# Optimization experiments

Hardware: AMD Instinct MI355X
Metric: run time of the kernel (lower is better)

## Reference

```python
import jax, jax.numpy as jnp
import numpy as np

B, S, D = 4, 2048, 1024
P = 2
N_FEAT = 16          # n_feature_know
N_REST = 16          # n_restore_know
R = 128              # knowledge_rank
D_SPACE = 64


def setup_inputs() -> dict:
    key = jax.random.key(0)
    ks = jax.random.split(key, 6)
    x = jax.random.normal(ks[0], (B, S, D), dtype=jnp.float32)
    # per-token routing weights for each of P feature paths, in [0,1)
    feature_paths = jax.random.uniform(ks[1], (P, B, S, N_FEAT), dtype=jnp.float32)
    f_know = jax.random.normal(ks[2], (N_FEAT, D, R), dtype=jnp.float32) * 0.02
    r_know = jax.random.normal(ks[3], (N_REST, R, D), dtype=jnp.float32) * 0.02
    feature_emb = jax.random.normal(ks[4], (N_FEAT, D_SPACE), dtype=jnp.float32)
    W_router = jax.random.normal(ks[5], (D_SPACE + R, N_REST), dtype=jnp.float32) * 0.05
    return {"x": x, "feature_paths": feature_paths, "f_know": f_know,
            "r_know": r_know, "feature_emb": feature_emb, "W_router": W_router}


def reference(x, feature_paths, f_know, r_know, feature_emb, W_router):
    # Feature projection into all N low-rank banks: [B,S,N,R]
    all_h = jnp.einsum('bsd,ndr->bsnr', x, f_know)
    # Weighted sum over banks per path: [P,B,S,R]
    h_all = jnp.einsum('bsnr,pbsn->pbsr', all_h, feature_paths)
    # Context for restore routing: [P,B,S,D_SPACE]
    neuron_ctx = jnp.einsum('pbsn,nd->pbsd', feature_paths, feature_emb)
    # restore_input = cat([neuron_ctx, h]) -> router -> softmax restore weights
    restore_input = jnp.concatenate([neuron_ctx, h_all], axis=-1)  # [P,B,S,D_SPACE+R]
    logits = jnp.einsum('pbsc,cn->pbsn', restore_input, W_router)
    w = jax.nn.softmax(logits, axis=-1)                            # [P,B,S,N_REST]
    # Restore + per-token weighted combine, summed over P paths: [B,S,D]
    output = jnp.einsum('pbsr,nrd,pbsn->bsd', h_all, r_know, w)
    restore_aux_loss = jnp.float32(0.0)
    return output, restore_aux_loss
```

## Files before the change

kernel.cpp:

```cpp
#include <hip/hip_runtime.h>

typedef __attribute__((ext_vector_type(4))) float f32x4;
typedef __bf16 bf16x8 __attribute__((ext_vector_type(8)));
typedef unsigned short ushort_t;

#define T_TOK 8192
#define DIM   1024
#define NRCOL 2048

#define VMW(n)  asm volatile("s_waitcnt vmcnt(" #n ")" ::: "memory")
#define SB0()   __builtin_amdgcn_sched_barrier(0)
#define BAR()   __builtin_amdgcn_s_barrier()

static __device__ __forceinline__ unsigned short f2bf(float f) {
  unsigned int u = __builtin_bit_cast(unsigned int, f);
  u += 0x7fffu + ((u >> 16) & 1u);
  return (unsigned short)(u >> 16);
}
static __device__ __forceinline__ float bfbits2f(unsigned int lo16) {
  return __builtin_bit_cast(float, lo16 << 16);
}
static __device__ __forceinline__ void gload16(const void* g, void* l) {
  __builtin_amdgcn_global_load_lds((const __attribute__((address_space(1))) void*)g,
                                   (__attribute__((address_space(3))) void*)l, 16, 0, 0);
}

__global__ __launch_bounds__(256) void cvt_f32_bf16(const float* __restrict__ in,
                                                    unsigned short* __restrict__ out,
                                                    int n4) {
  int i = blockIdx.x * 256 + threadIdx.x;
  const int stride = gridDim.x * 256;
  const float4* in4 = (const float4*)in;
  uint2* o4 = (uint2*)out;
  for (; i < n4; i += stride) {
    float4 v = in4[i];
    uint2 o;
    o.x = (unsigned)f2bf(v.x) | ((unsigned)f2bf(v.y) << 16);
    o.y = (unsigned)f2bf(v.z) | ((unsigned)f2bf(v.w) << 16);
    o4[i] = o;
  }
}

__global__ __launch_bounds__(256) void tcvt(const float* __restrict__ src,
                                            unsigned short* __restrict__ dst,
                                            int rows, int cols,
                                            long sstride, long dstride) {
  src += (size_t)blockIdx.z * sstride;
  dst += (size_t)blockIdx.z * dstride;
  __shared__ float tile[32][33];
  const int tx = threadIdx.x & 31, ty = threadIdx.x >> 5;
  const int r0 = blockIdx.y * 32, c0 = blockIdx.x * 32;
  #pragma unroll
  for (int i = 0; i < 32; i += 8)
    tile[ty + i][tx] = src[(size_t)(r0 + ty + i) * cols + c0 + tx];
  __syncthreads();
  #pragma unroll
  for (int i = 0; i < 32; i += 8)
    dst[(size_t)(c0 + ty + i) * rows + r0 + tx] = f2bf(tile[tx][ty + i]);
}

template<int BM, int BK, int K, bool OUT_BF16>
__global__ __launch_bounds__(512, 2) void gemmP(const ushort_t* __restrict__ A,
                                                const ushort_t* __restrict__ Bt,
                                                void* __restrict__ Cp, int N) {
  constexpr int nt = K / BK;
  constexpr int KS = BK / 32;
  constexpr int MF = BM / 32;
  constexpr int CH = BK / 8;
  constexpr int AR = BM * BK * 2 / 8192;
  constexpr int BR = 256 * BK * 2 / 8192;
  constexpr int LPT = AR + BR;
  __shared__ ushort_t As[3][BM * BK];
  __shared__ ushort_t Bs[3][256 * BK];

  const int tid = threadIdx.x;
  const int nx = gridDim.x;
  const int orig = blockIdx.y * nx + blockIdx.x;
  const int q = (nx * gridDim.y) >> 3;
  const int swz = (orig & 7) * q + (orig >> 3);
  const int bx = swz % nx, by = swz / nx;

  const int lane = tid & 63, wv = tid >> 6;
  const int wm = wv >> 2, wn = wv & 3;
  const int lrow = lane & 15, lk = lane >> 4;

  const ushort_t* Ab = A + (size_t)by * BM * K;
  const ushort_t* Bb = Bt + (size_t)bx * 256 * K;

  const int srow = tid * 16 / (BK * 2);
  const int sch = ((tid * 16 >> 4) & (CH - 1)) ^ (srow & (CH - 1));
  constexpr int RPR = 8192 / (BK * 2);
  const ushort_t* pA[AR];
  const ushort_t* pB[BR];
  #pragma unroll
  for (int r = 0; r < AR; ++r) pA[r] = Ab + (size_t)(r * RPR + srow) * K + sch * 8;
  #pragma unroll
  for (int r = 0; r < BR; ++r) pB[r] = Bb + (size_t)(r * RPR + srow) * K + sch * 8;
  const int dL = tid * 8;

  int oA[MF], oB[4];
  #pragma unroll
  for (int m = 0; m < MF; ++m) {
    const int r = wm * (BM / 2) + m * 16 + lrow;
    oA[m] = r * BK + (lk ^ (r & (CH - 1))) * 8;
  }
  #pragma unroll
  for (int n = 0; n < 4; ++n) {
    const int r = wn * 64 + n * 16 + lrow;
    oB[n] = r * BK + (lk ^ (r & (CH - 1))) * 8;
  }

  f32x4 acc[MF][4];
  #pragma unroll
  for (int m = 0; m < MF; ++m)
    #pragma unroll
    for (int n = 0; n < 4; ++n)
      acc[m][n] = (f32x4){0.f, 0.f, 0.f, 0.f};

  auto stage = [&](int s, int adv) {
    #pragma unroll
    for (int r = 0; r < AR; ++r) gload16(pA[r] + adv, (void*)&As[s][r * 4096 + dL]);
    #pragma unroll
    for (int r = 0; r < BR; ++r) gload16(pB[r] + adv, (void*)&Bs[s][r * 4096 + dL]);
  };

  stage(0, 0);
  stage(1, BK);
  if constexpr (LPT == 4) VMW(4); else VMW(6);
  SB0(); BAR(); SB0();

  bf16x8 av[2][MF][KS], bv01[2][KS], bv23[2][KS];
  #pragma unroll
  for (int m = 0; m < MF; ++m)
    #pragma unroll
    for (int ks = 0; ks < KS; ++ks)
      av[0][m][ks] = *(const bf16x8*)&As[0][oA[m] ^ (ks * 32)];
  #pragma unroll
  for (int n = 0; n < 2; ++n)
    #pragma unroll
    for (int ks = 0; ks < KS; ++ks)
      bv01[n][ks] = *(const bf16x8*)&Bs[0][oB[n] ^ (ks * 32)];

  #pragma unroll
  for (int t = 0; t < nt; ++t) {
    const int s = t % 3, s1 = (t + 1) % 3, s2 = (t + 2) % 3;
    const int p = t & 1;
    if (t + 2 < nt) stage(s2, (t + 2) * BK);
    #pragma unroll
    for (int n = 0; n < 2; ++n)
      #pragma unroll
      for (int ks = 0; ks < KS; ++ks)
        bv23[n][ks] = *(const bf16x8*)&Bs[s][oB[n + 2] ^ (ks * 32)];
    #pragma unroll
    for (int ks = 0; ks < KS; ++ks)
      #pragma unroll
      for (int m = 0; m < MF; ++m)
        #pragma unroll
        for (int n = 0; n < 2; ++n)
          acc[m][n] = __builtin_amdgcn_mfma_f32_16x16x32_bf16(av[p][m][ks], bv01[n][ks], acc[m][n], 0, 0, 0);
    SB0();
    if (t + 2 < nt) { if constexpr (LPT == 4) VMW(4); else VMW(6); }
    else            { VMW(0); }
    BAR(); SB0();
    if (t + 1 < nt) {
      #pragma unroll
      for (int m = 0; m < MF; ++m)
        #pragma unroll
        for (int ks = 0; ks < KS; ++ks)
          av[p ^ 1][m][ks] = *(const bf16x8*)&As[s1][oA[m] ^ (ks * 32)];
      #pragma unroll
      for (int n = 0; n < 2; ++n)
        #pragma unroll
        for (int ks = 0; ks < KS; ++ks)
          bv01[n][ks] = *(const bf16x8*)&Bs[s1][oB[n] ^ (ks * 32)];
    }
    #pragma unroll
    for (int ks = 0; ks < KS; ++ks)
      #pragma unroll
      for (int m = 0; m < MF; ++m)
        #pragma unroll
        for (int n = 0; n < 2; ++n)
          acc[m][n + 2] = __builtin_amdgcn_mfma_f32_16x16x32_bf16(av[p][m][ks], bv23[n][ks], acc[m][n + 2], 0, 0, 0);
    SB0(); BAR(); SB0();
  }

  #pragma unroll
  for (int m = 0; m < MF; ++m) {
    const int row0 = by * BM + wm * (BM / 2) + m * 16 + lk * 4;
    #pragma unroll
    for (int n = 0; n < 4; ++n) {
      const int col = bx * 256 + wn * 64 + n * 16 + lrow;
      #pragma unroll
      for (int j = 0; j < 4; ++j) {
        const size_t idx = (size_t)(row0 + j) * N + col;
        if constexpr (OUT_BF16) ((ushort_t*)Cp)[idx] = f2bf(acc[m][n][j]);
        else                    ((float*)Cp)[idx] = acc[m][n][j];
      }
    }
  }
}

__global__ __launch_bounds__(256) void middle_kernel(const unsigned short* __restrict__ AH,
                                                     const float* __restrict__ fp,
                                                     const float* __restrict__ femb,
                                                     const float* __restrict__ Wr,
                                                     unsigned short* __restrict__ Mout,
                                                     float* __restrict__ auxout) {
  __shared__ float G[16][16];
  __shared__ float hs[4][2][128];
  __shared__ float wsm[4][2][16];
  const int tid = threadIdx.x;
  {
    const int n = tid >> 4, j = tid & 15;
    float s = 0.f;
    #pragma unroll
    for (int ds = 0; ds < 64; ++ds) s += femb[n * 64 + ds] * Wr[ds * 16 + j];
    G[n][j] = s;
  }
  const int wv = tid >> 6, l = tid & 63;
  const int t = blockIdx.x * 4 + wv;

  float p0[16], p1[16];
  #pragma unroll
  for (int n = 0; n < 16; ++n) {
    p0[n] = fp[t * 16 + n];
    p1[n] = fp[T_TOK * 16 + t * 16 + n];
  }

  float h00 = 0.f, h01 = 0.f, h10 = 0.f, h11 = 0.f;
  const unsigned short* ahrow = AH + (size_t)t * NRCOL;
  #pragma unroll
  for (int n = 0; n < 16; ++n) {
    const unsigned int v = *(const unsigned int*)(ahrow + n * 128 + 2 * l);
    const float a0 = bfbits2f(v & 0xffffu);
    const float a1 = bfbits2f(v >> 16);
    h00 += a0 * p0[n]; h01 += a1 * p0[n];
    h10 += a0 * p1[n]; h11 += a1 * p1[n];
  }
  hs[wv][0][2 * l] = h00; hs[wv][0][2 * l + 1] = h01;
  hs[wv][1][2 * l] = h10; hs[wv][1][2 * l + 1] = h11;
  __syncthreads();

  if (l < 32) {
    const int p = l >> 4, j = l & 15;
    float s = 0.f;
    #pragma unroll
    for (int n = 0; n < 16; ++n) s += (p ? p1[n] : p0[n]) * G[n][j];
    const float* hp = hs[wv][p];
    const float* wr = Wr + 64 * 16 + j;
    float s0 = 0.f, s1 = 0.f, s2 = 0.f, s3 = 0.f;
    #pragma unroll
    for (int r = 0; r < 128; r += 4) {
      s0 += hp[r]     * wr[(r)     * 16];
      s1 += hp[r + 1] * wr[(r + 1) * 16];
      s2 += hp[r + 2] * wr[(r + 2) * 16];
      s3 += hp[r + 3] * wr[(r + 3) * 16];
    }
    s += (s0 + s1) + (s2 + s3);
    float mx = s;
    #pragma unroll
    for (int d = 1; d < 16; d <<= 1) mx = fmaxf(mx, __shfl_xor(mx, d, 64));
    const float e = __expf(s - mx);
    float sum = e;
    #pragma unroll
    for (int d = 1; d < 16; d <<= 1) sum += __shfl_xor(sum, d, 64);
    wsm[wv][p][j] = e / sum;
  }
  __syncthreads();

  unsigned short* mrow = Mout + (size_t)t * NRCOL;
  #pragma unroll
  for (int n = 0; n < 16; ++n) {
    const float w0 = wsm[wv][0][n], w1 = wsm[wv][1][n];
    const float m0 = w0 * h00 + w1 * h10;
    const float m1 = w0 * h01 + w1 * h11;
    const unsigned int pk = (unsigned)f2bf(m0) | ((unsigned)f2bf(m1) << 16);
    *(unsigned int*)(mrow + n * 128 + 2 * l) = pk;
  }
  if (blockIdx.x == 0 && tid == 0) auxout[0] = 0.f;
}

extern "C" void kernel_launch(void* const* d_in, const int* in_sizes, int n_in,
                              void* d_out, int out_size, void* d_ws, size_t ws_size,
                              hipStream_t stream) {
  const float* x    = (const float*)d_in[0];
  const float* fp   = (const float*)d_in[1];
  const float* fk   = (const float*)d_in[2];
  const float* rk   = (const float*)d_in[3];
  const float* femb = (const float*)d_in[4];
  const float* Wr   = (const float*)d_in[5];
  float* out = (float*)d_out;

  char* ws = (char*)d_ws;
  unsigned short* Xbf = (unsigned short*)ws;
  unsigned short* W1t = (unsigned short*)(ws + 16u * 1024 * 1024);
  unsigned short* Mb  = (unsigned short*)ws;
  unsigned short* W2t = (unsigned short*)(ws + 32u * 1024 * 1024);
  unsigned short* AH  = (unsigned short*)(ws + 36u * 1024 * 1024);

  cvt_f32_bf16<<<2048, 256, 0, stream>>>(x, Xbf, (T_TOK * DIM) / 4);
  tcvt<<<dim3(128 / 32, 1024 / 32, 16), 256, 0, stream>>>(fk, W1t, 1024, 128,
                                                          1024L * 128, 128L * 1024);
  tcvt<<<dim3(1024 / 32, 2048 / 32, 1), 256, 0, stream>>>(rk, W2t, 2048, 1024, 0, 0);
  gemmP<256, 32, 1024, true><<<dim3(NRCOL / 256, T_TOK / 256), 512, 0, stream>>>(Xbf, W1t, AH, NRCOL);
  middle_kernel<<<T_TOK / 4, 256, 0, stream>>>(AH, fp, femb, Wr, Mb, out + 8388608);
  gemmP<128, 64, 2048, false><<<dim3(DIM / 256, T_TOK / 128), 512, 0, stream>>>(Mb, W2t, out, DIM);
}
```

Before: 115.9 us.

## Fuse prep conversions into one kernel, retile first GEMM, parallelize router logits

Merges the x bf16 conversion and the two weight transpose-conversions into a single prep kernel launch, which removes two launch gaps. Switches the first GEMM tile from BM=256/BK=32 to BM=128/BK=64, doubling its grid for better occupancy and load balance. In the middle kernel, the router weights are staged in shared memory and all 64 lanes compute the logits, with the rank dimension split across two half-wavefronts and combined by a shuffle instead of only 32 lanes reading global memory. The cost is extra shared memory and a larger preload per block in the middle kernel.

```diff
diff --git a/kernel.cpp b/kernel.cpp
--- a/kernel.cpp
+++ b/kernel.cpp
@@ -25,31 +25,45 @@
                                    (__attribute__((address_space(3))) void*)l, 16, 0, 0);
 }
 
-__global__ __launch_bounds__(256) void cvt_f32_bf16(const float* __restrict__ in,
-                                                    unsigned short* __restrict__ out,
-                                                    int n4) {
-  int i = blockIdx.x * 256 + threadIdx.x;
-  const int stride = gridDim.x * 256;
-  const float4* in4 = (const float4*)in;
-  uint2* o4 = (uint2*)out;
-  for (; i < n4; i += stride) {
-    float4 v = in4[i];
-    uint2 o;
-    o.x = (unsigned)f2bf(v.x) | ((unsigned)f2bf(v.y) << 16);
-    o.y = (unsigned)f2bf(v.z) | ((unsigned)f2bf(v.w) << 16);
-    o4[i] = o;
-  }
-}
-
-__global__ __launch_bounds__(256) void tcvt(const float* __restrict__ src,
-                                            unsigned short* __restrict__ dst,
-                                            int rows, int cols,
-                                            long sstride, long dstride) {
-  src += (size_t)blockIdx.z * sstride;
-  dst += (size_t)blockIdx.z * dstride;
+__global__ __launch_bounds__(256) void prep_kernel(const float* __restrict__ x,
+                                                   const float* __restrict__ fk,
+                                                   const float* __restrict__ rk,
+                                                   unsigned short* __restrict__ Xbf,
+                                                   unsigned short* __restrict__ W1t,
+                                                   unsigned short* __restrict__ W2t) {
+  const int bid = blockIdx.x, tid = threadIdx.x;
+  if (bid < 2048) {
+    const float4* in4 = (const float4*)x;
+    uint2* o4 = (uint2*)Xbf;
+    #pragma unroll
+    for (int it = 0; it < 4; ++it) {
+      const int i = bid * 256 + tid + it * 524288;
+      float4 v = in4[i];
+      uint2 o;
+      o.x = (unsigned)f2bf(v.x) | ((unsigned)f2bf(v.y) << 16);
+      o.y = (unsigned)f2bf(v.z) | ((unsigned)f2bf(v.w) << 16);
+      o4[i] = o;
+    }
+    return;
+  }
   __shared__ float tile[32][33];
-  const int tx = threadIdx.x & 31, ty = threadIdx.x >> 5;
-  const int r0 = blockIdx.y * 32, c0 = blockIdx.x * 32;
+  const float* src;
+  unsigned short* dst;
+  int rows, cols, r0, c0;
+  if (bid < 4096) {
+    const int b = bid - 2048;
+    const int z = b >> 7, rem = b & 127;
+    src = fk + (size_t)z * 1024 * 128;
+    dst = W1t + (size_t)z * 128 * 1024;
+    rows = 1024; cols = 128;
+    c0 = (rem & 3) * 32; r0 = (rem >> 2) * 32;
+  } else {
+    const int b = bid - 4096;
+    src = rk; dst = W2t;
+    rows = 2048; cols = 1024;
+    c0 = (b & 31) * 32; r0 = (b >> 5) * 32;
+  }
+  const int tx = tid & 31, ty = tid >> 5;
   #pragma unroll
   for (int i = 0; i < 32; i += 8)
     tile[ty + i][tx] = src[(size_t)(r0 + ty + i) * cols + c0 + tx];
@@ -207,6 +221,7 @@
                                                      unsigned short* __restrict__ Mout,
                                                      float* __restrict__ auxout) {
   __shared__ float G[16][16];
+  __shared__ float WrBs[128 * 16];
   __shared__ float hs[4][2][128];
   __shared__ float wsm[4][2][16];
   const int tid = threadIdx.x;
@@ -216,6 +231,9 @@
     #pragma unroll
     for (int ds = 0; ds < 64; ++ds) s += femb[n * 64 + ds] * Wr[ds * 16 + j];
     G[n][j] = s;
+    #pragma unroll
+    for (int k = 0; k < 8; ++k)
+      WrBs[tid * 8 + k] = Wr[64 * 16 + tid * 8 + k];
   }
   const int wv = tid >> 6, l = tid & 63;
   const int t = blockIdx.x * 4 + wv;
@@ -241,22 +259,25 @@
   hs[wv][1][2 * l] = h10; hs[wv][1][2 * l + 1] = h11;
   __syncthreads();
 
-  if (l < 32) {
-    const int p = l >> 4, j = l & 15;
-    float s = 0.f;
-    #pragma unroll
-    for (int n = 0; n < 16; ++n) s += (p ? p1[n] : p0[n]) * G[n][j];
-    const float* hp = hs[wv][p];
-    const float* wr = Wr + 64 * 16 + j;
+  {
+    const int p = l >> 5, seg = (l >> 4) & 1, j = l & 15;
+    const float* hp = hs[wv][p] + seg * 64;
+    const float* wb = WrBs + seg * 64 * 16 + j;
     float s0 = 0.f, s1 = 0.f, s2 = 0.f, s3 = 0.f;
     #pragma unroll
-    for (int r = 0; r < 128; r += 4) {
-      s0 += hp[r]     * wr[(r)     * 16];
-      s1 += hp[r + 1] * wr[(r + 1) * 16];
-      s2 += hp[r + 2] * wr[(r + 2) * 16];
-      s3 += hp[r + 3] * wr[(r + 3) * 16];
-    }
-    s += (s0 + s1) + (s2 + s3);
+    for (int r = 0; r < 64; r += 4) {
+      s0 += hp[r]     * wb[(r)     * 16];
+      s1 += hp[r + 1] * wb[(r + 1) * 16];
+      s2 += hp[r + 2] * wb[(r + 2) * 16];
+      s3 += hp[r + 3] * wb[(r + 3) * 16];
+    }
+    float s = (s0 + s1) + (s2 + s3);
+    s += __shfl_xor(s, 16, 64);
+    #pragma unroll
+    for (int n = 0; n < 16; ++n) {
+      const float fv = p ? p1[n] : p0[n];
+      s += fv * G[n][j];
+    }
     float mx = s;
     #pragma unroll
     for (int d = 1; d < 16; d <<= 1) mx = fmaxf(mx, __shfl_xor(mx, d, 64));
@@ -264,7 +285,7 @@
     float sum = e;
     #pragma unroll
     for (int d = 1; d < 16; d <<= 1) sum += __shfl_xor(sum, d, 64);
-    wsm[wv][p][j] = e / sum;
+    if (seg == 0) wsm[wv][p][j] = e / sum;
   }
   __syncthreads();
 
@@ -298,11 +319,8 @@
   unsigned short* W2t = (unsigned short*)(ws + 32u * 1024 * 1024);
   unsigned short* AH  = (unsigned short*)(ws + 36u * 1024 * 1024);
 
-  cvt_f32_bf16<<<2048, 256, 0, stream>>>(x, Xbf, (T_TOK * DIM) / 4);
-  tcvt<<<dim3(128 / 32, 1024 / 32, 16), 256, 0, stream>>>(fk, W1t, 1024, 128,
-                                                          1024L * 128, 128L * 1024);
-  tcvt<<<dim3(1024 / 32, 2048 / 32, 1), 256, 0, stream>>>(rk, W2t, 2048, 1024, 0, 0);
-  gemmP<256, 32, 1024, true><<<dim3(NRCOL / 256, T_TOK / 256), 512, 0, stream>>>(Xbf, W1t, AH, NRCOL);
+  prep_kernel<<<6144, 256, 0, stream>>>(x, fk, rk, Xbf, W1t, W2t);
+  gemmP<128, 64, 1024, true><<<dim3(NRCOL / 256, T_TOK / 128), 512, 0, stream>>>(Xbf, W1t, AH, NRCOL);
   middle_kernel<<<T_TOK / 4, 256, 0, stream>>>(AH, fp, femb, Wr, Mb, out + 8388608);
   gemmP<128, 64, 2048, false><<<dim3(DIM / 256, T_TOK / 128), 512, 0, stream>>>(Mb, W2t, out, DIM);
 }
```

Measured after the change: 110.5 us. 1.05x faster.
